# Optimization experiments

Measured on AMD Instinct MI355X. Metric: run time of the kernel, lower is better.

Reference implementation:

```python
import jax, jax.numpy as jnp
import numpy as np

B, N, D, H = 2, 4096, 256, 8
HD = D // H
NEG_SLOPE = 0.01
LN_EPS = 1e-5


def setup_inputs() -> dict:
    key = jax.random.key(0)
    ks = jax.random.split(key, 6)
    s = 1.0 / np.sqrt(D)
    return {
        "h": jax.random.normal(ks[0], (B, N, D), dtype=jnp.float32),
        "W_l": jax.random.normal(ks[1], (D, D), dtype=jnp.float32) * s,
        "W_r": jax.random.normal(ks[2], (D, D), dtype=jnp.float32) * s,
        "a_l": jax.random.normal(ks[3], (HD,), dtype=jnp.float32) * s,
        "a_r": jax.random.normal(ks[4], (HD,), dtype=jnp.float32) * s,
        "W_final": jax.random.normal(ks[5], (D, D), dtype=jnp.float32) * s,
        "ln_g": jnp.ones((D,), dtype=jnp.float32),
        "ln_b": jnp.zeros((D,), dtype=jnp.float32),
    }


def _leaky(x):
    return jnp.where(x >= 0, x, NEG_SLOPE * x)


def reference(h, W_l, W_r, a_l, a_r, W_final, ln_g, ln_b):
    b, n, d = h.shape
    # projections -> [b, H, n, HD]
    fl = (h @ W_l).reshape(b, n, H, HD).transpose(0, 2, 1, 3)
    fr = (h @ W_r).reshape(b, n, H, HD).transpose(0, 2, 1, 3)
    # additive GAT-style scores: [b, H, n] each, broadcast to [b, H, n, n]
    sl = jnp.einsum("bhnd,d->bhn", _leaky(fl), a_l)
    sr = jnp.einsum("bhnd,d->bhn", _leaky(fr), a_r)
    score = sl[..., :, None] + sr[..., None, :]  # [b, H, n, n]
    attn = jnp.mean(score, axis=1)  # pre-softmax mean over heads: [b, n, n]
    p = jax.nn.softmax(score, axis=-1)  # dropout is identity (eval / p=0)
    context = jnp.einsum("bhij,bhjd->bhid", p, fr)  # [b, H, n, HD]
    h_sa = context.transpose(0, 2, 1, 3).reshape(b, n, d)
    fh = h_sa @ W_final
    x = h + fh
    mu = jnp.mean(x, axis=-1, keepdims=True)
    var = jnp.mean(jnp.square(x - mu), axis=-1, keepdims=True)
    h_out = (x - mu) * jax.lax.rsqrt(var + LN_EPS) * ln_g + ln_b
    return (h_out, attn)
```

## Files before the change

### kernel.cpp

```cpp
#include <hip/hip_runtime.h>
#include <hip/hip_bf16.h>

#define BATCH 2
#define SEQ   4096
#define DIM   256
#define HEADS 8
#define HDIM  32
#define M_ROWS (BATCH * SEQ)
#define FPSCALE 4294967296.0
#define ATTNROWS 4
#define ATTNBLKS (M_ROWS / ATTNROWS)

typedef short bf16x8 __attribute__((ext_vector_type(8)));
typedef unsigned short u16x8 __attribute__((ext_vector_type(8)));
typedef float f32x4 __attribute__((ext_vector_type(4)));

static __device__ inline unsigned short f2bf(float x) {
  union { float f; unsigned u; } v; v.f = x;
  unsigned r = v.u + 0x7FFF + ((v.u >> 16) & 1);
  return (unsigned short)(r >> 16);
}

__global__ __launch_bounds__(256) void k_prep(const float* __restrict__ Wl,
                                              const float* __restrict__ Wr,
                                              unsigned short* __restrict__ Wt,
                                              unsigned long long* __restrict__ yctx,
                                              unsigned long long* __restrict__ wacc) {
  if (blockIdx.y == 0) {
    const int idx = blockIdx.x * 256 + threadIdx.x;
    if (idx < BATCH * DIM) yctx[idx] = 0ull;
    if (idx < BATCH * HEADS) wacc[idx] = 0ull;
  }
  __shared__ float tile[32][33];
  const int k0 = blockIdx.x * 32;
  const int n0 = blockIdx.y * 32;
  const int t = threadIdx.x;
  const float* W = (n0 < 256) ? Wl : Wr;
  const int nb = n0 & 255;
  {
    const int r = t >> 3;
    const int c = (t & 7) * 4;
    const float4 v = *(const float4*)(&W[(size_t)(k0 + r) * DIM + nb + c]);
    tile[r][c + 0] = v.x; tile[r][c + 1] = v.y;
    tile[r][c + 2] = v.z; tile[r][c + 3] = v.w;
  }
  __syncthreads();
  {
    const int nl = t >> 3;
    const int kl = (t & 7) * 4;
    ushort4 o;
    o.x = f2bf(tile[kl + 0][nl]); o.y = f2bf(tile[kl + 1][nl]);
    o.z = f2bf(tile[kl + 2][nl]); o.w = f2bf(tile[kl + 3][nl]);
    *(ushort4*)(&Wt[(size_t)(n0 + nl) * DIM + k0 + kl]) = o;
  }
}

__global__ __launch_bounds__(512) void k_gemm_fused(
    const float* __restrict__ A, const unsigned short* __restrict__ Wt,
    const float* __restrict__ a_l, const float* __restrict__ a_r,
    float* __restrict__ msl, float* __restrict__ msr,
    unsigned long long* __restrict__ yctx,
    unsigned long long* __restrict__ wacc) {
  __shared__ unsigned short As[64 * 32];
  __shared__ unsigned short Bs[256 * 32];
  __shared__ float red[64][8];

  const int bid = blockIdx.x;
  const int isR = bid & 1;
  const int bm  = bid >> 1;
  const int m0 = bm * 64;
  const int n0 = isR * 256;

  const int t = threadIdx.x;
  const int lane = t & 63;
  const int wid = t >> 6;

  f32x4 acc[4][2];
  #pragma unroll
  for (int i = 0; i < 4; ++i)
    #pragma unroll
    for (int j = 0; j < 2; ++j) acc[i][j] = (f32x4){0.f, 0.f, 0.f, 0.f};

  for (int k0 = 0; k0 < DIM; k0 += 32) {
    if (t < 256) {
      const int row = t >> 2;
      const int kc = t & 3;
      const int slot = kc ^ ((row >> 1) & 3);
      const float4 a0 = *(const float4*)(&A[(size_t)(m0 + row) * DIM + k0 + kc * 8]);
      const float4 a1 = *(const float4*)(&A[(size_t)(m0 + row) * DIM + k0 + kc * 8 + 4]);
      u16x8 pa;
      pa[0] = f2bf(a0.x); pa[1] = f2bf(a0.y); pa[2] = f2bf(a0.z); pa[3] = f2bf(a0.w);
      pa[4] = f2bf(a1.x); pa[5] = f2bf(a1.y); pa[6] = f2bf(a1.z); pa[7] = f2bf(a1.w);
      *(u16x8*)((char*)As + row * 64 + slot * 16) = pa;
    }
    #pragma unroll
    for (int p = 0; p < 2; ++p) {
      const int task = t + p * 512;
      const int row = task >> 2;
      const int kc = task & 3;
      const int slot = kc ^ ((row >> 1) & 3);
      const u16x8 pb = *(const u16x8*)(&Wt[(size_t)(n0 + row) * DIM + k0 + kc * 8]);
      *(u16x8*)((char*)Bs + row * 64 + slot * 16) = pb;
    }
    __syncthreads();

    bf16x8 af[4], bfr[2];
    #pragma unroll
    for (int mr = 0; mr < 4; ++mr) {
      const int ra = mr * 16 + (lane & 15);
      const int sl = (lane >> 4) ^ ((ra >> 1) & 3);
      af[mr] = *(const bf16x8*)((const char*)As + ra * 64 + sl * 16);
    }
    #pragma unroll
    for (int nr = 0; nr < 2; ++nr) {
      const int cb = wid * 32 + nr * 16 + (lane & 15);
      const int sl = (lane >> 4) ^ ((cb >> 1) & 3);
      bfr[nr] = *(const bf16x8*)((const char*)Bs + cb * 64 + sl * 16);
    }
    #pragma unroll
    for (int mr = 0; mr < 4; ++mr)
      #pragma unroll
      for (int nr = 0; nr < 2; ++nr)
        acc[mr][nr] = __builtin_amdgcn_mfma_f32_16x16x32_bf16(af[mr], bfr[nr], acc[mr][nr], 0, 0, 0);
    __syncthreads();
  }

  const float* av = isR ? a_r : a_l;
  const int b = m0 >> 12;

  float e[4][4];
  #pragma unroll
  for (int mr = 0; mr < 4; ++mr) {
    #pragma unroll
    for (int r = 0; r < 4; ++r) {
      float p = 0.f;
      #pragma unroll
      for (int nr = 0; nr < 2; ++nr) {
        float x = acc[mr][nr][r];
        x = x >= 0.f ? x : 0.01f * x;
        p = fmaf(x, av[nr * 16 + (lane & 15)], p);
      }
      #pragma unroll
      for (int o = 1; o < 16; o <<= 1) p += __shfl_xor(p, o, 16);
      if ((lane & 15) == 0) {
        const int rl = mr * 16 + (lane >> 4) * 4 + r;
        red[rl][wid] = p;
      }
      e[mr][r] = __expf(p);
    }
  }

  if (isR) {
    float se = 0.f;
    #pragma unroll
    for (int mr = 0; mr < 4; ++mr)
      #pragma unroll
      for (int r = 0; r < 4; ++r) se += e[mr][r];
    se += __shfl_xor(se, 16, 64);
    se += __shfl_xor(se, 32, 64);
    if (lane == 0)
      atomicAdd(&wacc[b * HEADS + wid],
                (unsigned long long)__double2ll_rn((double)se * FPSCALE));
    #pragma unroll
    for (int nr = 0; nr < 2; ++nr) {
      float y = 0.f;
      #pragma unroll
      for (int mr = 0; mr < 4; ++mr)
        #pragma unroll
        for (int r = 0; r < 4; ++r)
          y = fmaf(e[mr][r], acc[mr][nr][r], y);
      y += __shfl_xor(y, 16, 64);
      y += __shfl_xor(y, 32, 64);
      if (lane < 16)
        atomicAdd(&yctx[(size_t)b * DIM + wid * 32 + nr * 16 + lane],
                  (unsigned long long)__double2ll_rn((double)y * FPSCALE));
    }
  }
  __syncthreads();
  if (t < 64) {
    float s = 0.f;
    #pragma unroll
    for (int h2 = 0; h2 < 8; ++h2) s += red[t][h2];
    (isR ? msr : msl)[m0 + t] = s * 0.125f;
  }
}

__global__ __launch_bounds__(256) void k_attn_fh(
    const float* __restrict__ msl, const float* __restrict__ msr,
    const unsigned long long* __restrict__ yctx,
    const unsigned long long* __restrict__ wacc,
    const float* __restrict__ Wf,
    float* __restrict__ fh2, float* __restrict__ attn) {
  const int blk = blockIdx.x;
  const int t = threadIdx.x;

  if (blk < BATCH) {
    const int b = blk;
    __shared__ float c_s[DIM];
    c_s[t] = (float)((double)(long long)yctx[(size_t)b * DIM + t] /
                     (double)(long long)wacc[b * HEADS + (t >> 5)]);
    __syncthreads();
    float a2 = 0.f;
    #pragma unroll 8
    for (int k = 0; k < DIM; ++k)
      a2 = fmaf(c_s[k], Wf[(size_t)k * DIM + t], a2);
    fh2[b * DIM + t] = a2;
    return;
  }

  const int row0 = (blk - BATCH) * ATTNROWS;
  const int b = row0 >> 12;
  f32x4 m[4];
  const f32x4* mr4 = (const f32x4*)(msr + ((size_t)b << 12));
  #pragma unroll
  for (int q = 0; q < 4; ++q) m[q] = mr4[q * 256 + t];
  #pragma unroll
  for (int rr = 0; rr < ATTNROWS; ++rr) {
    const float v = msl[row0 + rr];
    f32x4* dst = (f32x4*)(attn + ((size_t)(row0 + rr) << 12));
    #pragma unroll
    for (int q = 0; q < 4; ++q)
      __builtin_nontemporal_store(m[q] + v, &dst[q * 256 + t]);
  }
}

__global__ __launch_bounds__(256) void k_ln(const float* __restrict__ h,
                                            const float* __restrict__ fh2,
                                            const float* __restrict__ g,
                                            const float* __restrict__ bb,
                                            float* __restrict__ out) {
  const int row0 = blockIdx.x * 2;
  const int b = row0 >> 12;
  const int t = threadIdx.x;

  const float fh = fh2[b * DIM + t];
  const float x0 = h[(size_t)row0 * DIM + t] + fh;
  const float x1 = h[(size_t)(row0 + 1) * DIM + t] + fh;
  float s10 = x0, s20 = x0 * x0, s11 = x1, s21 = x1 * x1;
  #pragma unroll
  for (int o = 32; o > 0; o >>= 1) {
    s10 += __shfl_xor(s10, o, 64);
    s20 += __shfl_xor(s20, o, 64);
    s11 += __shfl_xor(s11, o, 64);
    s21 += __shfl_xor(s21, o, 64);
  }
  __shared__ float r1[2][4], r2[2][4];
  if ((t & 63) == 0) {
    r1[0][t >> 6] = s10; r2[0][t >> 6] = s20;
    r1[1][t >> 6] = s11; r2[1][t >> 6] = s21;
  }
  __syncthreads();
  const float gs = g[t], bs = bb[t];
  {
    const float s1 = r1[0][0] + r1[0][1] + r1[0][2] + r1[0][3];
    const float s2 = r2[0][0] + r2[0][1] + r2[0][2] + r2[0][3];
    const float mu = s1 * (1.f / 256.f);
    const float var = s2 * (1.f / 256.f) - mu * mu;
    const float rs = rsqrtf(var + 1e-5f);
    out[(size_t)row0 * DIM + t] = (x0 - mu) * rs * gs + bs;
  }
  {
    const float s1 = r1[1][0] + r1[1][1] + r1[1][2] + r1[1][3];
    const float s2 = r2[1][0] + r2[1][1] + r2[1][2] + r2[1][3];
    const float mu = s1 * (1.f / 256.f);
    const float var = s2 * (1.f / 256.f) - mu * mu;
    const float rs = rsqrtf(var + 1e-5f);
    out[(size_t)(row0 + 1) * DIM + t] = (x1 - mu) * rs * gs + bs;
  }
}

extern "C" void kernel_launch(void* const* d_in, const int* in_sizes, int n_in,
                              void* d_out, int out_size, void* d_ws, size_t ws_size,
                              hipStream_t stream) {
  const float* h  = (const float*)d_in[0];
  const float* Wl = (const float*)d_in[1];
  const float* Wr = (const float*)d_in[2];
  const float* al = (const float*)d_in[3];
  const float* ar = (const float*)d_in[4];
  const float* Wf = (const float*)d_in[5];
  const float* g  = (const float*)d_in[6];
  const float* bb = (const float*)d_in[7];
  float* out = (float*)d_out;

  unsigned long long* yctx = (unsigned long long*)d_ws;
  unsigned long long* wacc = yctx + BATCH * DIM;
  float* msl = (float*)(wacc + BATCH * HEADS);
  float* msr = msl + M_ROWS;
  float* fh2 = msr + M_ROWS;
  unsigned short* Wt = (unsigned short*)(fh2 + BATCH * DIM);

  k_prep<<<dim3(8, 16), 256, 0, stream>>>(Wl, Wr, Wt, yctx, wacc);
  k_gemm_fused<<<256, 512, 0, stream>>>(h, Wt, al, ar, msl, msr, yctx, wacc);
  k_attn_fh<<<BATCH + ATTNBLKS, 256, 0, stream>>>(msl, msr, yctx, wacc, Wf,
                                                  fh2, out + (size_t)M_ROWS * DIM);
  k_ln<<<M_ROWS / 2, 256, 0, stream>>>(h, fh2, g, bb, out);
}
```

Measured before the change: 59.68 us.

## Fold final projection into last GEMM block and merge attn/LN kernels

The small context·W_final product moves into the GEMM kernel and runs in whichever block finishes last, detected with an atomic completion counter. The attention-broadcast and layernorm kernels are merged into one launch. Together these cut the pipeline from four launches to three and remove the serial dependency in which the LN blocks waited on a separate kernel. The cost is that one block does a 256x256 matvec serially at the tail of the GEMM, and correctness relies on atomic reads for memory visibility without an explicit fence.

```diff
diff --git a/kernel.cpp b/kernel.cpp
--- a/kernel.cpp
+++ b/kernel.cpp
@@ -10,6 +10,7 @@
 #define FPSCALE 4294967296.0
 #define ATTNROWS 4
 #define ATTNBLKS (M_ROWS / ATTNROWS)
+#define LNBLKS (M_ROWS / 2)
 
 typedef short bf16x8 __attribute__((ext_vector_type(8)));
 typedef unsigned short u16x8 __attribute__((ext_vector_type(8)));
@@ -25,11 +26,13 @@
                                               const float* __restrict__ Wr,
                                               unsigned short* __restrict__ Wt,
                                               unsigned long long* __restrict__ yctx,
-                                              unsigned long long* __restrict__ wacc) {
+                                              unsigned long long* __restrict__ wacc,
+                                              unsigned* __restrict__ ctr) {
   if (blockIdx.y == 0) {
     const int idx = blockIdx.x * 256 + threadIdx.x;
     if (idx < BATCH * DIM) yctx[idx] = 0ull;
     if (idx < BATCH * HEADS) wacc[idx] = 0ull;
+    if (idx == 0) *ctr = 0u;
   }
   __shared__ float tile[32][33];
   const int k0 = blockIdx.x * 32;
@@ -58,12 +61,17 @@
 __global__ __launch_bounds__(512) void k_gemm_fused(
     const float* __restrict__ A, const unsigned short* __restrict__ Wt,
     const float* __restrict__ a_l, const float* __restrict__ a_r,
+    const float* __restrict__ Wf,
     float* __restrict__ msl, float* __restrict__ msr,
     unsigned long long* __restrict__ yctx,
-    unsigned long long* __restrict__ wacc) {
+    unsigned long long* __restrict__ wacc,
+    unsigned* __restrict__ ctr,
+    float* __restrict__ fh2) {
   __shared__ unsigned short As[64 * 32];
   __shared__ unsigned short Bs[256 * 32];
   __shared__ float red[64][8];
+  __shared__ float c_sh[BATCH * DIM];
+  __shared__ unsigned done_s;
 
   const int bid = blockIdx.x;
   const int isR = bid & 1;
@@ -183,56 +191,57 @@
     for (int h2 = 0; h2 < 8; ++h2) s += red[t][h2];
     (isR ? msr : msl)[m0 + t] = s * 0.125f;
   }
-}
-
-__global__ __launch_bounds__(256) void k_attn_fh(
-    const float* __restrict__ msl, const float* __restrict__ msr,
-    const unsigned long long* __restrict__ yctx,
-    const unsigned long long* __restrict__ wacc,
-    const float* __restrict__ Wf,
-    float* __restrict__ fh2, float* __restrict__ attn) {
-  const int blk = blockIdx.x;
-  const int t = threadIdx.x;
-
-  if (blk < BATCH) {
-    const int b = blk;
-    __shared__ float c_s[DIM];
-    c_s[t] = (float)((double)(long long)yctx[(size_t)b * DIM + t] /
-                     (double)(long long)wacc[b * HEADS + (t >> 5)]);
+
+  if (t == 0) done_s = atomicAdd(ctr, 1u);
+  __syncthreads();
+  if (done_s == 255u) {
+    {
+      const int b2 = t >> 8, d = t & 255;
+      const unsigned long long yv = atomicAdd(&yctx[t], 0ull);
+      const unsigned long long wv = atomicAdd(&wacc[b2 * HEADS + (d >> 5)], 0ull);
+      c_sh[t] = (float)((double)(long long)yv / (double)(long long)wv);
+    }
     __syncthreads();
+    const int b2 = t >> 8, n = t & 255;
     float a2 = 0.f;
     #pragma unroll 8
     for (int k = 0; k < DIM; ++k)
-      a2 = fmaf(c_s[k], Wf[(size_t)k * DIM + t], a2);
-    fh2[b * DIM + t] = a2;
+      a2 = fmaf(c_sh[b2 * DIM + k], Wf[(size_t)k * DIM + n], a2);
+    fh2[b2 * DIM + n] = a2;
+  }
+}
+
+__global__ __launch_bounds__(256) void k_out(const float* __restrict__ h,
+                                             const float* __restrict__ fh2,
+                                             const float* __restrict__ g,
+                                             const float* __restrict__ bb,
+                                             const float* __restrict__ msl,
+                                             const float* __restrict__ msr,
+                                             float* __restrict__ out,
+                                             float* __restrict__ attn) {
+  const int blk = blockIdx.x;
+  const int t = threadIdx.x;
+
+  if (blk < ATTNBLKS) {
+    const int row0 = blk * ATTNROWS;
+    const int b = row0 >> 12;
+    f32x4 m[4];
+    const f32x4* mr4 = (const f32x4*)(msr + ((size_t)b << 12));
+    #pragma unroll
+    for (int q = 0; q < 4; ++q) m[q] = mr4[q * 256 + t];
+    #pragma unroll
+    for (int rr = 0; rr < ATTNROWS; ++rr) {
+      const float v = msl[row0 + rr];
+      f32x4* dst = (f32x4*)(attn + ((size_t)(row0 + rr) << 12));
+      #pragma unroll
+      for (int q = 0; q < 4; ++q)
+        __builtin_nontemporal_store(m[q] + v, &dst[q * 256 + t]);
+    }
     return;
   }
 
-  const int row0 = (blk - BATCH) * ATTNROWS;
+  const int row0 = (blk - ATTNBLKS) * 2;
   const int b = row0 >> 12;
-  f32x4 m[4];
-  const f32x4* mr4 = (const f32x4*)(msr + ((size_t)b << 12));
-  #pragma unroll
-  for (int q = 0; q < 4; ++q) m[q] = mr4[q * 256 + t];
-  #pragma unroll
-  for (int rr = 0; rr < ATTNROWS; ++rr) {
-    const float v = msl[row0 + rr];
-    f32x4* dst = (f32x4*)(attn + ((size_t)(row0 + rr) << 12));
-    #pragma unroll
-    for (int q = 0; q < 4; ++q)
-      __builtin_nontemporal_store(m[q] + v, &dst[q * 256 + t]);
-  }
-}
-
-__global__ __launch_bounds__(256) void k_ln(const float* __restrict__ h,
-                                            const float* __restrict__ fh2,
-                                            const float* __restrict__ g,
-                                            const float* __restrict__ bb,
-                                            float* __restrict__ out) {
-  const int row0 = blockIdx.x * 2;
-  const int b = row0 >> 12;
-  const int t = threadIdx.x;
-
   const float fh = fh2[b * DIM + t];
   const float x0 = h[(size_t)row0 * DIM + t] + fh;
   const float x1 = h[(size_t)(row0 + 1) * DIM + t] + fh;
@@ -284,14 +293,16 @@
 
   unsigned long long* yctx = (unsigned long long*)d_ws;
   unsigned long long* wacc = yctx + BATCH * DIM;
-  float* msl = (float*)(wacc + BATCH * HEADS);
+  unsigned long long* ctrq = wacc + BATCH * HEADS;
+  unsigned* ctr = (unsigned*)ctrq;
+  float* msl = (float*)(ctrq + 1);
   float* msr = msl + M_ROWS;
   float* fh2 = msr + M_ROWS;
   unsigned short* Wt = (unsigned short*)(fh2 + BATCH * DIM);
 
-  k_prep<<<dim3(8, 16), 256, 0, stream>>>(Wl, Wr, Wt, yctx, wacc);
-  k_gemm_fused<<<256, 512, 0, stream>>>(h, Wt, al, ar, msl, msr, yctx, wacc);
-  k_attn_fh<<<BATCH + ATTNBLKS, 256, 0, stream>>>(msl, msr, yctx, wacc, Wf,
-                                                  fh2, out + (size_t)M_ROWS * DIM);
-  k_ln<<<M_ROWS / 2, 256, 0, stream>>>(h, fh2, g, bb, out);
-}
+  k_prep<<<dim3(8, 16), 256, 0, stream>>>(Wl, Wr, Wt, yctx, wacc, ctr);
+  k_gemm_fused<<<256, 512, 0, stream>>>(h, Wt, al, ar, Wf, msl, msr,
+                                        yctx, wacc, ctr, fh2);
+  k_out<<<ATTNBLKS + LNBLKS, 256, 0, stream>>>(h, fh2, g, bb, msl, msr,
+                                               out, out + (size_t)M_ROWS * DIM);
+}
```

Result: slower. 62.01 us (+3.9%).
